# Kernel optimization log

Hardware: AMD Instinct MI355X
Metric: run time of the kernel (lower is better)

Reference implementation:

```python
import jax, jax.numpy as jnp
import numpy as np

BIAS = 1.0
SIGMA = 0.5
EPS = 1e-5


def mrf_loss(gen, target):
    # gen, target: [B, C, H, W]
    mean_t = jnp.mean(target, axis=1, keepdims=True)
    gf = gen - mean_t
    tf = target - mean_t
    gn = gf / jnp.linalg.norm(gf, axis=1, keepdims=True)
    tn = tf / jnp.linalg.norm(tf, axis=1, keepdims=True)
    B, C, H, W = target.shape
    # 1x1 patches of target, ordered by spatial position (matches unfold h,w order)
    patches = tn.transpose(0, 2, 3, 1).reshape(B, H * W, C)  # [B, P, C]
    # per-sample conv2d with 1x1 kernels == batched GEMM
    sim = jnp.einsum('bpc,bchw->bphw', patches, gn)  # [B, P, H, W]
    cosine_dist = -(sim - 1.0) / 2.0
    relative = cosine_dist / (jnp.min(cosine_dist, axis=1, keepdims=True) + EPS)
    dist = jnp.exp((BIAS - relative) / SIGMA)
    cs = dist / jnp.sum(dist, axis=1, keepdims=True)
    k_max = jnp.max(cs.reshape(B, H * W, -1), axis=2)  # [B, P]
    div_mrf = jnp.mean(k_max, axis=1)  # [B]
    return jnp.sum(-jnp.log(div_mrf))


def setup_inputs() -> dict:
    key = jax.random.key(0)
    k1, k2, k3, k4 = jax.random.split(key, 4)
    return {
        'gen_relu3_2': jax.random.normal(k1, (4, 256, 64, 64), dtype=jnp.float32),
        'tar_relu3_2': jax.random.normal(k2, (4, 256, 64, 64), dtype=jnp.float32),
        'gen_relu4_2': jax.random.normal(k3, (4, 512, 32, 32), dtype=jnp.float32),
        'tar_relu4_2': jax.random.normal(k4, (4, 512, 32, 32), dtype=jnp.float32),
    }


def reference(gen_relu3_2, tar_relu3_2, gen_relu4_2, tar_relu4_2):
    # style layers: relu3_2 (w=1.0), relu4_2 (w=1.0); content layers: relu4_2 (w=1.0)
    m3 = mrf_loss(gen_relu3_2, tar_relu3_2)
    m4 = mrf_loss(gen_relu4_2, tar_relu4_2)
    style_loss = (1.0 * m3 + 1.0 * m4) * 1.0  # l_s = 1.0
    content_loss = (1.0 * m4) * 1.0           # l_c = 1.0
    return style_loss + content_loss
```

## Files before the change

kernel.cpp:

```cpp
#include <hip/hip_runtime.h>
#include <math.h>


#define MRF_EPS 1e-5f
#define LOG2E 1.44269504088896340736f

typedef __attribute__((ext_vector_type(8))) short bf16x8;
typedef __attribute__((ext_vector_type(4))) float f32x4;
typedef unsigned short ushort_t;
struct __align__(8) ushort4_t { ushort_t x, y, z, w; };
struct __align__(16) ushort8_t { ushort_t v[8]; };

__device__ __forceinline__ ushort_t f2bf(float x) {
    unsigned u = __float_as_uint(x);
    u += 0x7FFFu + ((u >> 16) & 1u);
    return (ushort_t)(u >> 16);
}
__device__ __forceinline__ float bf2f(ushort_t u) {
    return __uint_as_float(((unsigned)u) << 16);
}

typedef __attribute__((address_space(1))) const unsigned int gu32;
typedef __attribute__((address_space(3))) unsigned int lu32;
__device__ __forceinline__ void gload16(const ushort_t* g, ushort_t* l) {
    __builtin_amdgcn_global_load_lds((gu32*)(uintptr_t)g, (lu32*)(uintptr_t)l,
                                     16, 0, 0);
}

__global__ __launch_bounds__(256) void stats_all(
    const float* __restrict__ gen3, const float* __restrict__ tar3,
    const float* __restrict__ gen4, const float* __restrict__ tar4,
    float* __restrict__ mean3, float* __restrict__ rg3, float* __restrict__ rt3,
    float* __restrict__ mean4, float* __restrict__ rg4, float* __restrict__ rt4) {
    const float *gen, *tar; float *mean, *rg, *rt; int C, S, b, bx;
    int bid = blockIdx.x;
    if (bid < 256) {
        C = 512; S = 1024; b = bid >> 6; bx = bid & 63;
        gen = gen4; tar = tar4; mean = mean4; rg = rg4; rt = rt4;
    } else {
        bid -= 256;
        C = 256; S = 4096; b = bid >> 8; bx = bid & 255;
        gen = gen3; tar = tar3; mean = mean3; rg = rg3; rt = rt3;
    }
    int tid = threadIdx.x, pq = tid & 3, cs = tid >> 2;
    int s0 = bx * 16 + pq * 4;
    const float* g = gen + (size_t)b * C * S + s0;
    const float* t = tar + (size_t)b * C * S + s0;

    f32x4 st = {0.f, 0.f, 0.f, 0.f}, st2 = st, sg = st, sg2 = st;
    for (int c = cs; c < C; c += 64) {
        f32x4 tv = *(const f32x4*)(t + (size_t)c * S);
        f32x4 gv = *(const f32x4*)(g + (size_t)c * S);
        st += tv; st2 += tv * tv; sg += gv; sg2 += gv * gv;
    }
    __shared__ f32x4 red[4][4][64];
    __shared__ f32x4 red2[4][4][4];
    red[0][pq][cs] = st; red[1][pq][cs] = st2; red[2][pq][cs] = sg; red[3][pq][cs] = sg2;
    __syncthreads();
    if (tid < 64) {
        int s_ = tid >> 4, p_ = (tid >> 2) & 3, part = tid & 3;
        f32x4 s = red[s_][p_][part * 16];
#pragma unroll
        for (int j = 1; j < 16; j++) s += red[s_][p_][part * 16 + j];
        red2[s_][p_][part] = s;
    }
    __syncthreads();
    if (tid < 4) {
        f32x4 sts = red2[0][tid][0] + red2[0][tid][1] + red2[0][tid][2] + red2[0][tid][3];
        f32x4 st2s = red2[1][tid][0] + red2[1][tid][1] + red2[1][tid][2] + red2[1][tid][3];
        f32x4 sgs = red2[2][tid][0] + red2[2][tid][1] + red2[2][tid][2] + red2[2][tid][3];
        f32x4 sg2s = red2[3][tid][0] + red2[3][tid][1] + red2[3][tid][2] + red2[3][tid][3];
        f32x4 m, vrt, vrg;
        float invC = 1.f / (float)C;
#pragma unroll
        for (int e = 0; e < 4; e++) {
            float mm = sts[e] * invC;
            m[e] = mm;
            vrt[e] = rsqrtf(st2s[e] - mm * sts[e]);
            vrg[e] = rsqrtf(sg2s[e] - 2.f * mm * sgs[e] + mm * sts[e]);
        }
        int idx = b * S + bx * 16 + tid * 4;
        *(f32x4*)(mean + idx) = m;
        *(f32x4*)(rt + idx) = vrt;
        *(f32x4*)(rg + idx) = vrg;
    }
}

__global__ __launch_bounds__(256) void apply_all(
    const float* __restrict__ gen3, const float* __restrict__ tar3,
    const float* __restrict__ gen4, const float* __restrict__ tar4,
    const float* __restrict__ mean3, const float* __restrict__ rg3, const float* __restrict__ rt3,
    const float* __restrict__ mean4, const float* __restrict__ rg4, const float* __restrict__ rt4,
    ushort_t* __restrict__ gnT3, ushort_t* __restrict__ tnT3,
    ushort_t* __restrict__ gnT4, ushort_t* __restrict__ tnT4) {
    const float *gen, *tar, *mean, *rg, *rt; ushort_t *gnT, *tnT;
    int C, S, b, sxb, cyb;
    int bid = blockIdx.x;
    if (bid < 512) {
        C = 512; S = 1024; b = bid >> 7; int rem = bid & 127;
        cyb = rem >> 4; sxb = rem & 15;
        gen = gen4; tar = tar4; mean = mean4; rg = rg4; rt = rt4; gnT = gnT4; tnT = tnT4;
    } else {
        bid -= 512;
        C = 256; S = 4096; b = bid >> 8; int rem = bid & 255;
        cyb = rem >> 6; sxb = rem & 63;
        gen = gen3; tar = tar3; mean = mean3; rg = rg3; rt = rt3; gnT = gnT3; tnT = tnT3;
    }
    int tid = threadIdx.x;
    int s0 = sxb * 64, c0 = cyb * 64;
    const float* g = gen + (size_t)b * C * S;
    const float* t = tar + (size_t)b * C * S;
    int tx = tid & 63, tw = tid >> 6;
    int sidx = b * S + s0 + tx;
    float m = mean[sidx], rgv = rg[sidx], rtv = rt[sidx];

    __shared__ ushort_t tg[64][72], tt_[64][72];
#pragma unroll
    for (int i = 0; i < 16; i++) {
        int cl = tw * 16 + i;
        float gv = g[(size_t)(c0 + cl) * S + s0 + tx];
        float tv = t[(size_t)(c0 + cl) * S + s0 + tx];
        tg[tx][cl] = f2bf((gv - m) * rgv);
        tt_[tx][cl] = f2bf((tv - m) * rtv);
    }
    __syncthreads();
    int KC = C >> 3;
#pragma unroll
    for (int j = 0; j < 2; j++) {
        int p = j * 256 + tid;
        int s = p & 63, ch = p >> 6;
        int row = s0 + s;
        int r16 = row >> 4, lm = row & 15;
        size_t off = (size_t)b * S * C + (((size_t)r16 * KC + (c0 >> 3) + ch) * 16 + lm) * 8;
        *(ushort8_t*)(gnT + off) = *(const ushort8_t*)&tg[s][ch * 8];
        *(ushort8_t*)(tnT + off) = *(const ushort8_t*)&tt_[s][ch * 8];
    }
}

template <int K>
__device__ __forceinline__ void gemm_body(
    const ushort_t* __restrict__ A, const ushort_t* __restrict__ B,
    ushort_t* __restrict__ sim, float* __restrict__ cmPart,
    int S, int bx, int by, ushort_t* __restrict__ lds) {
    const int tid = threadIdx.x;
    const int lane = tid & 63, wave = tid >> 6;
    const int wm = (wave & 1) * 64, wn = (wave >> 1) * 64;
    const int lm = lane & 15, quad = lane >> 4;
    const int q0 = bx * 128;

    constexpr int KC = K / 8;
    constexpr int KB = K / 32;

    const ushort_t* segsrc[4];
    ushort_t* segdst[4];
#pragma unroll
    for (int i = 0; i < 4; i++) {
        int s = wave * 4 + i;
        segsrc[i] = (s < 8)
            ? A + ((size_t)(by * 8 + s) * KC) * 128 + lane * 8
            : B + ((size_t)(bx * 8 + (s - 8)) * KC) * 128 + lane * 8;
        segdst[i] = lds + s * 512;
    }

    auto stage = [&](int buf, int kb) {
#pragma unroll
        for (int i = 0; i < 4; i++)
            gload16(segsrc[i] + (size_t)kb * 512, segdst[i] + buf * 8192);
    };

    f32x4 acc[4][4];
#pragma unroll
    for (int t = 0; t < 4; t++)
#pragma unroll
        for (int u = 0; u < 4; u++) acc[t][u] = (f32x4){0.f, 0.f, 0.f, 0.f};

    stage(0, 0);
    stage(1, 1);
    asm volatile("s_waitcnt vmcnt(4)" ::: "memory");
    __builtin_amdgcn_s_barrier();

    const ushort_t* lA = lds + (wm >> 4) * 512 + quad * 128 + lm * 8;
    const ushort_t* lB = lds + 4096 + (wn >> 4) * 512 + quad * 128 + lm * 8;

#pragma unroll
    for (int kb = 0; kb < KB; kb++) {
        const int cur = (kb % 3) * 8192;
        if (kb + 2 < KB) stage((kb + 2) % 3, kb + 2);
        bf16x8 a[4], b[4];
#pragma unroll
        for (int t = 0; t < 4; t++) {
            a[t] = *(const bf16x8*)(lA + cur + t * 512);
            b[t] = *(const bf16x8*)(lB + cur + t * 512);
        }
        asm volatile("s_waitcnt lgkmcnt(0)" ::: "memory");
        __builtin_amdgcn_sched_barrier(0);
#pragma unroll
        for (int t = 0; t < 4; t++)
#pragma unroll
            for (int u = 0; u < 4; u++)
                acc[t][u] = __builtin_amdgcn_mfma_f32_16x16x32_bf16(a[t], b[u], acc[t][u], 0, 0, 0);
        if (kb + 1 < KB) {
            if (kb + 2 < KB) asm volatile("s_waitcnt vmcnt(4)" ::: "memory");
            else             asm volatile("s_waitcnt vmcnt(0)" ::: "memory");
            __builtin_amdgcn_s_barrier();
        }
    }

    int nQB = S >> 7;
    size_t base = ((size_t)(by * nQB + bx)) * 16384
                + (size_t)(wave * 4096 + quad * 64 + lm * 4);
    float cmax[4] = {-INFINITY, -INFINITY, -INFINITY, -INFINITY};
#pragma unroll
    for (int t = 0; t < 4; t++)
#pragma unroll
        for (int u = 0; u < 4; u++) {
            f32x4 v = acc[t][u];
            ushort4_t o;
            o.x = f2bf(v.x); o.y = f2bf(v.y); o.z = f2bf(v.z); o.w = f2bf(v.w);
            *(ushort4_t*)(sim + base + (t * 4 + u) * 256) = o;
            float mx = fmaxf(fmaxf(bf2f(o.x), bf2f(o.y)), fmaxf(bf2f(o.z), bf2f(o.w)));
            cmax[u] = fmaxf(cmax[u], mx);
        }
    int r = by * 2 + (wave & 1);
#pragma unroll
    for (int u = 0; u < 4; u++) {
        float m = cmax[u];
        m = fmaxf(m, __shfl_xor(m, 16, 64));
        m = fmaxf(m, __shfl_xor(m, 32, 64));
        if (lane < 16) cmPart[(size_t)r * S + q0 + wn + u * 16 + lane] = m;
    }
}

__global__ __launch_bounds__(256) void gemm_all(
    const ushort_t* __restrict__ tnT3, const ushort_t* __restrict__ gnT3,
    ushort_t* __restrict__ sim3, float* __restrict__ cmPart3,
    const ushort_t* __restrict__ tnT4, const ushort_t* __restrict__ gnT4,
    ushort_t* __restrict__ sim4, float* __restrict__ cmPart4) {
    __shared__ ushort_t lds[24576];
    int bid = blockIdx.x;
    if (bid < 256) {
        int z = bid >> 6, rem = bid & 63, by = rem >> 3, bx = rem & 7;
        gemm_body<512>(tnT4 + (size_t)z * 524288, gnT4 + (size_t)z * 524288,
                       sim4 + (size_t)z * 1048576, cmPart4 + (size_t)z * 16384,
                       1024, bx, by, lds);
    } else {
        bid -= 256;
        int z = bid >> 10, rem = bid & 1023, by = rem >> 5, bx = rem & 31;
        gemm_body<256>(tnT3 + (size_t)z * 1048576, gnT3 + (size_t)z * 1048576,
                       sim3 + (size_t)z * 16777216, cmPart3 + (size_t)z * 262144,
                       4096, bx, by, lds);
    }
}

__global__ __launch_bounds__(256) void colmax_reduce_all(
    const float* __restrict__ cmPart3, float2* __restrict__ coef3, float* __restrict__ colsum3,
    const float* __restrict__ cmPart4, float2* __restrict__ coef4, float* __restrict__ colsum4,
    float* __restrict__ acc) {
    const float* cmPart; float2* coef; float* colsum; int S, R, qb, accIdx;
    int bid = blockIdx.x;
    if (bid < 16) {
        int z = bid >> 2; qb = bid & 3; S = 1024; R = 16; accIdx = 4 + z;
        cmPart = cmPart4 + (size_t)z * 16384; coef = coef4 + (size_t)z * 1024;
        colsum = colsum4 + (size_t)z * 1024;
    } else {
        bid -= 16;
        int z = bid >> 4; qb = bid & 15; S = 4096; R = 64; accIdx = z;
        cmPart = cmPart3 + (size_t)z * 262144; coef = coef3 + (size_t)z * 4096;
        colsum = colsum3 + (size_t)z * 4096;
    }
    if (qb == 0 && threadIdx.x == 0) acc[accIdx] = 0.f;
    int q = qb * 256 + threadIdx.x;
    float m = cmPart[q];
    for (int r = 1; r < R; r++) m = fmaxf(m, cmPart[(size_t)r * S + q]);
    float c1 = 1.f / ((1.f - m) * 0.5f + MRF_EPS);
    coef[q] = make_float2((2.f - c1) * LOG2E, c1 * LOG2E);
    colsum[q] = 0.f;
}

__global__ __launch_bounds__(256) void colsum_all(
    const ushort_t* __restrict__ sim3, const float2* __restrict__ coef3, float* __restrict__ colsum3,
    const ushort_t* __restrict__ sim4, const float2* __restrict__ coef4, float* __restrict__ colsum4) {
    const ushort_t* sim; const float2* coef; float* colsum; int S, bx, by;
    int bid = blockIdx.x;
    if (bid < 256) {
        int z = bid >> 6, rem = bid & 63; by = rem >> 3; bx = rem & 7; S = 1024;
        sim = sim4 + (size_t)z * 1048576; coef = coef4 + (size_t)z * 1024;
        colsum = colsum4 + (size_t)z * 1024;
    } else {
        bid -= 256;
        int z = bid >> 10, rem = bid & 1023; by = rem >> 5; bx = rem & 31; S = 4096;
        sim = sim3 + (size_t)z * 16777216; coef = coef3 + (size_t)z * 4096;
        colsum = colsum3 + (size_t)z * 4096;
    }
    int tid = threadIdx.x, lane = tid & 63;
    int u = lane >> 4, lm = lane & 15;
    int sub = (tid >> 6) & 1, cg = tid >> 7;
    int nQB = S >> 7;
    int q = bx * 128 + cg * 64 + u * 16 + lm;
    float2 cc = coef[q];
    float c0 = cc.x, c1 = cc.y;
    const ushort_t* base = sim + ((size_t)(by * nQB + bx)) * 16384
                         + (size_t)((sub | (cg << 1)) * 4096 + u * 256 + lm * 4);
    float s = 0.f;
#pragma unroll
    for (int t = 0; t < 4; t++)
#pragma unroll
        for (int quad = 0; quad < 4; quad++) {
            ushort4_t w = *(const ushort4_t*)(base + t * 1024 + quad * 64);
            s += exp2f(c0 + c1 * bf2f(w.x)) + exp2f(c0 + c1 * bf2f(w.y))
               + exp2f(c0 + c1 * bf2f(w.z)) + exp2f(c0 + c1 * bf2f(w.w));
        }
    atomicAdd(colsum + q, s);
}

__global__ __launch_bounds__(256) void rowmax_all(
    const ushort_t* __restrict__ sim3, const float2* __restrict__ coef3, const float* __restrict__ colsum3,
    const ushort_t* __restrict__ sim4, const float2* __restrict__ coef4, const float* __restrict__ colsum4,
    float* __restrict__ acc) {
    const ushort_t* sim; const float2* coef; const float* colsum;
    int S, blk; float* accSlot;
    int bid = blockIdx.x;
    if (bid < 1024) {
        int z = bid >> 8; blk = bid & 255; S = 4096; accSlot = acc + z;
        sim = sim3 + (size_t)z * 16777216; coef = coef3 + (size_t)z * 4096;
        colsum = colsum3 + (size_t)z * 4096;
    } else {
        bid -= 1024;
        int z = bid >> 6; blk = bid & 63; S = 1024; accSlot = acc + 4 + z;
        sim = sim4 + (size_t)z * 1048576; coef = coef4 + (size_t)z * 1024;
        colsum = colsum4 + (size_t)z * 1024;
    }
    int wave = threadIdx.x >> 6, lane = threadIdx.x & 63;
    int g = blk * 4 + wave;
    int by = g >> 5, rem = g & 31;
    int sub = rem >> 4, t = (rem >> 2) & 3, quad = rem & 3;
    int u = lane >> 4, lm = lane & 15;
    int nQB = S >> 7;
    f32x4 m = {-INFINITY, -INFINITY, -INFINITY, -INFINITY};
    for (int bx = 0; bx < nQB; bx++) {
#pragma unroll
        for (int cg = 0; cg < 2; cg++) {
            int q = bx * 128 + cg * 64 + u * 16 + lm;
            float2 cc = coef[q];
            float c0p = cc.x - log2f(colsum[q]);
            const ushort_t* ptr = sim + ((size_t)(by * nQB + bx)) * 16384
                                + (size_t)((sub | (cg << 1)) * 4096 + (t * 4 + u) * 256 + quad * 64 + lm * 4);
            ushort4_t w = *(const ushort4_t*)ptr;
            m[0] = fmaxf(m[0], c0p + cc.y * bf2f(w.x));
            m[1] = fmaxf(m[1], c0p + cc.y * bf2f(w.y));
            m[2] = fmaxf(m[2], c0p + cc.y * bf2f(w.z));
            m[3] = fmaxf(m[3], c0p + cc.y * bf2f(w.w));
        }
    }
#pragma unroll
    for (int off = 32; off >= 1; off >>= 1)
#pragma unroll
        for (int e = 0; e < 4; e++)
            m[e] = fmaxf(m[e], __shfl_xor(m[e], off, 64));
    __shared__ float partial[4];
    if (lane == 0)
        partial[wave] = exp2f(m[0]) + exp2f(m[1]) + exp2f(m[2]) + exp2f(m[3]);
    __syncthreads();
    if (threadIdx.x == 0)
        atomicAdd(accSlot, partial[0] + partial[1] + partial[2] + partial[3]);
}

__global__ void finalize_kernel(const float* __restrict__ acc, float* __restrict__ out) {
    float loss = 0.f;
    for (int b = 0; b < 4; b++) loss += -logf(acc[b] * (1.f / 4096.f));
    for (int b = 0; b < 4; b++) loss += -2.f * logf(acc[4 + b] * (1.f / 1024.f));
    out[0] = loss;
}

extern "C" void kernel_launch(void* const* d_in, const int* in_sizes, int n_in,
                              void* d_out, int out_size, void* d_ws, size_t ws_size,
                              hipStream_t stream) {
    const float* gen3 = (const float*)d_in[0];
    const float* tar3 = (const float*)d_in[1];
    const float* gen4 = (const float*)d_in[2];
    const float* tar4 = (const float*)d_in[3];

    char* wsb = (char*)d_ws;
    size_t off = 0;
    auto alloc = [&](size_t bytes) {
        void* p = wsb + off;
        off += (bytes + 255) & ~(size_t)255;
        return p;
    };
    ushort_t* sim3 = (ushort_t*)alloc((size_t)4 * 16777216 * 2);
    ushort_t* gnT3 = (ushort_t*)alloc((size_t)4 * 1048576 * 2);
    ushort_t* tnT3 = (ushort_t*)alloc((size_t)4 * 1048576 * 2);
    float* cmPart3 = (float*)alloc((size_t)4 * 262144 * 4);
    float2* coef3 = (float2*)alloc((size_t)4 * 4096 * 8);
    float* colsum3 = (float*)alloc((size_t)4 * 4096 * 4);
    float* mean3 = (float*)alloc((size_t)4 * 4096 * 4);
    float* rg3 = (float*)alloc((size_t)4 * 4096 * 4);
    float* rt3 = (float*)alloc((size_t)4 * 4096 * 4);
    ushort_t* sim4 = (ushort_t*)alloc((size_t)4 * 1048576 * 2);
    ushort_t* gnT4 = (ushort_t*)alloc((size_t)4 * 524288 * 2);
    ushort_t* tnT4 = (ushort_t*)alloc((size_t)4 * 524288 * 2);
    float* cmPart4 = (float*)alloc((size_t)4 * 16384 * 4);
    float2* coef4 = (float2*)alloc((size_t)4 * 1024 * 8);
    float* colsum4 = (float*)alloc((size_t)4 * 1024 * 4);
    float* mean4 = (float*)alloc((size_t)4 * 1024 * 4);
    float* rg4 = (float*)alloc((size_t)4 * 1024 * 4);
    float* rt4 = (float*)alloc((size_t)4 * 1024 * 4);
    float* acc = (float*)alloc(64 * 4);

    stats_all<<<256 + 1024, 256, 0, stream>>>(
        gen3, tar3, gen4, tar4, mean3, rg3, rt3, mean4, rg4, rt4);
    apply_all<<<512 + 1024, 256, 0, stream>>>(
        gen3, tar3, gen4, tar4, mean3, rg3, rt3, mean4, rg4, rt4,
        gnT3, tnT3, gnT4, tnT4);
    gemm_all<<<256 + 4096, 256, 0, stream>>>(
        tnT3, gnT3, sim3, cmPart3, tnT4, gnT4, sim4, cmPart4);
    colmax_reduce_all<<<16 + 64, 256, 0, stream>>>(
        cmPart3, coef3, colsum3, cmPart4, coef4, colsum4, acc);
    colsum_all<<<256 + 4096, 256, 0, stream>>>(
        sim3, coef3, colsum3, sim4, coef4, colsum4);
    rowmax_all<<<1024 + 256, 256, 0, stream>>>(
        sim3, coef3, colsum3, sim4, coef4, colsum4, acc);
    finalize_kernel<<<1, 1, 0, stream>>>(acc, (float*)d_out);
}
```

Before: 228.1 us.

## Recompute similarity GEMM in fused epilogues instead of materializing sim matrix

Removes the bf16 similarity buffer and instead reruns the batched GEMM three times: for column max, for the softmax column sums, and for per-tile row maxima. Row maxima go to a partial buffer that a small reduce kernel combines. This trades the large HBM write and two full re-reads of the similarity matrix for two extra passes of MFMA compute and on-chip epilogue work. Rounding to bf16 is kept so the values match the previous path.

Result: slower. 273.1 us (+19.7%).

```diff
diff --git a/kernel.cpp b/kernel.cpp
--- a/kernel.cpp
+++ b/kernel.cpp
@@ -19,6 +19,7 @@
 __device__ __forceinline__ float bf2f(ushort_t u) {
     return __uint_as_float(((unsigned)u) << 16);
 }
+__device__ __forceinline__ float rndbf(float x) { return bf2f(f2bf(x)); }
 
 typedef __attribute__((address_space(1))) const unsigned int gu32;
 typedef __attribute__((address_space(3))) unsigned int lu32;
@@ -138,15 +139,13 @@
 }
 
 template <int K>
-__device__ __forceinline__ void gemm_body(
+__device__ __forceinline__ void gemm_core(
     const ushort_t* __restrict__ A, const ushort_t* __restrict__ B,
-    ushort_t* __restrict__ sim, float* __restrict__ cmPart,
-    int S, int bx, int by, ushort_t* __restrict__ lds) {
+    int bx, int by, ushort_t* __restrict__ lds, f32x4 (&acc)[4][4]) {
     const int tid = threadIdx.x;
     const int lane = tid & 63, wave = tid >> 6;
     const int wm = (wave & 1) * 64, wn = (wave >> 1) * 64;
     const int lm = lane & 15, quad = lane >> 4;
-    const int q0 = bx * 128;
 
     constexpr int KC = K / 8;
     constexpr int KB = K / 32;
@@ -168,7 +167,6 @@
             gload16(segsrc[i] + (size_t)kb * 512, segdst[i] + buf * 8192);
     };
 
-    f32x4 acc[4][4];
 #pragma unroll
     for (int t = 0; t < 4; t++)
 #pragma unroll
@@ -205,20 +203,20 @@
             __builtin_amdgcn_s_barrier();
         }
     }
-
-    int nQB = S >> 7;
-    size_t base = ((size_t)(by * nQB + bx)) * 16384
-                + (size_t)(wave * 4096 + quad * 64 + lm * 4);
+}
+
+__device__ __forceinline__ void epilogueA(
+    f32x4 (&acc)[4][4], float* __restrict__ cmPart, int S, int bx, int by) {
+    int tid = threadIdx.x, lane = tid & 63, wave = tid >> 6;
+    int wn = (wave >> 1) * 64;
+    int q0 = bx * 128;
     float cmax[4] = {-INFINITY, -INFINITY, -INFINITY, -INFINITY};
 #pragma unroll
     for (int t = 0; t < 4; t++)
 #pragma unroll
         for (int u = 0; u < 4; u++) {
             f32x4 v = acc[t][u];
-            ushort4_t o;
-            o.x = f2bf(v.x); o.y = f2bf(v.y); o.z = f2bf(v.z); o.w = f2bf(v.w);
-            *(ushort4_t*)(sim + base + (t * 4 + u) * 256) = o;
-            float mx = fmaxf(fmaxf(bf2f(o.x), bf2f(o.y)), fmaxf(bf2f(o.z), bf2f(o.w)));
+            float mx = fmaxf(fmaxf(rndbf(v.x), rndbf(v.y)), fmaxf(rndbf(v.z), rndbf(v.w)));
             cmax[u] = fmaxf(cmax[u], mx);
         }
     int r = by * 2 + (wave & 1);
@@ -231,24 +229,23 @@
     }
 }
 
-__global__ __launch_bounds__(256) void gemm_all(
+__global__ __launch_bounds__(256) void gemmA_all(
     const ushort_t* __restrict__ tnT3, const ushort_t* __restrict__ gnT3,
-    ushort_t* __restrict__ sim3, float* __restrict__ cmPart3,
+    float* __restrict__ cmPart3,
     const ushort_t* __restrict__ tnT4, const ushort_t* __restrict__ gnT4,
-    ushort_t* __restrict__ sim4, float* __restrict__ cmPart4) {
+    float* __restrict__ cmPart4) {
     __shared__ ushort_t lds[24576];
+    f32x4 acc[4][4];
     int bid = blockIdx.x;
     if (bid < 256) {
         int z = bid >> 6, rem = bid & 63, by = rem >> 3, bx = rem & 7;
-        gemm_body<512>(tnT4 + (size_t)z * 524288, gnT4 + (size_t)z * 524288,
-                       sim4 + (size_t)z * 1048576, cmPart4 + (size_t)z * 16384,
-                       1024, bx, by, lds);
+        gemm_core<512>(tnT4 + (size_t)z * 524288, gnT4 + (size_t)z * 524288, bx, by, lds, acc);
+        epilogueA(acc, cmPart4 + (size_t)z * 16384, 1024, bx, by);
     } else {
         bid -= 256;
         int z = bid >> 10, rem = bid & 1023, by = rem >> 5, bx = rem & 31;
-        gemm_body<256>(tnT3 + (size_t)z * 1048576, gnT3 + (size_t)z * 1048576,
-                       sim3 + (size_t)z * 16777216, cmPart3 + (size_t)z * 262144,
-                       4096, bx, by, lds);
+        gemm_core<256>(tnT3 + (size_t)z * 1048576, gnT3 + (size_t)z * 1048576, bx, by, lds, acc);
+        epilogueA(acc, cmPart3 + (size_t)z * 262144, 4096, bx, by);
     }
 }
 
@@ -277,92 +274,157 @@
     colsum[q] = 0.f;
 }
 
-__global__ __launch_bounds__(256) void colsum_all(
-    const ushort_t* __restrict__ sim3, const float2* __restrict__ coef3, float* __restrict__ colsum3,
-    const ushort_t* __restrict__ sim4, const float2* __restrict__ coef4, float* __restrict__ colsum4) {
-    const ushort_t* sim; const float2* coef; float* colsum; int S, bx, by;
+__device__ __forceinline__ void epilogueB(
+    f32x4 (&acc)[4][4], const float2* __restrict__ coef,
+    float* __restrict__ colsum, int bx) {
+    int tid = threadIdx.x, lane = tid & 63, wave = tid >> 6;
+    int wn = (wave >> 1) * 64, lm = lane & 15;
+    int qb = bx * 128 + wn + lm;
+    float c0[4], c1[4], su[4];
+#pragma unroll
+    for (int u = 0; u < 4; u++) {
+        float2 cc = coef[qb + u * 16];
+        c0[u] = cc.x; c1[u] = cc.y; su[u] = 0.f;
+    }
+#pragma unroll
+    for (int t = 0; t < 4; t++)
+#pragma unroll
+        for (int u = 0; u < 4; u++) {
+            f32x4 v = acc[t][u];
+            su[u] += exp2f(c0[u] + c1[u] * rndbf(v.x));
+            su[u] += exp2f(c0[u] + c1[u] * rndbf(v.y));
+            su[u] += exp2f(c0[u] + c1[u] * rndbf(v.z));
+            su[u] += exp2f(c0[u] + c1[u] * rndbf(v.w));
+        }
+#pragma unroll
+    for (int u = 0; u < 4; u++) {
+        su[u] += __shfl_xor(su[u], 16, 64);
+        su[u] += __shfl_xor(su[u], 32, 64);
+        if (lane < 16) atomicAdd(colsum + qb + u * 16, su[u]);
+    }
+}
+
+__global__ __launch_bounds__(256) void gemmB_all(
+    const ushort_t* __restrict__ tnT3, const ushort_t* __restrict__ gnT3,
+    const float2* __restrict__ coef3, float* __restrict__ colsum3,
+    const ushort_t* __restrict__ tnT4, const ushort_t* __restrict__ gnT4,
+    const float2* __restrict__ coef4, float* __restrict__ colsum4) {
+    __shared__ ushort_t lds[24576];
+    f32x4 acc[4][4];
     int bid = blockIdx.x;
     if (bid < 256) {
-        int z = bid >> 6, rem = bid & 63; by = rem >> 3; bx = rem & 7; S = 1024;
-        sim = sim4 + (size_t)z * 1048576; coef = coef4 + (size_t)z * 1024;
-        colsum = colsum4 + (size_t)z * 1024;
+        int z = bid >> 6, rem = bid & 63, by = rem >> 3, bx = rem & 7;
+        gemm_core<512>(tnT4 + (size_t)z * 524288, gnT4 + (size_t)z * 524288, bx, by, lds, acc);
+        epilogueB(acc, coef4 + (size_t)z * 1024, colsum4 + (size_t)z * 1024, bx);
     } else {
         bid -= 256;
-        int z = bid >> 10, rem = bid & 1023; by = rem >> 5; bx = rem & 31; S = 4096;
-        sim = sim3 + (size_t)z * 16777216; coef = coef3 + (size_t)z * 4096;
-        colsum = colsum3 + (size_t)z * 4096;
-    }
-    int tid = threadIdx.x, lane = tid & 63;
-    int u = lane >> 4, lm = lane & 15;
-    int sub = (tid >> 6) & 1, cg = tid >> 7;
-    int nQB = S >> 7;
-    int q = bx * 128 + cg * 64 + u * 16 + lm;
-    float2 cc = coef[q];
-    float c0 = cc.x, c1 = cc.y;
-    const ushort_t* base = sim + ((size_t)(by * nQB + bx)) * 16384
-                         + (size_t)((sub | (cg << 1)) * 4096 + u * 256 + lm * 4);
-    float s = 0.f;
+        int z = bid >> 10, rem = bid & 1023, by = rem >> 5, bx = rem & 31;
+        gemm_core<256>(tnT3 + (size_t)z * 1048576, gnT3 + (size_t)z * 1048576, bx, by, lds, acc);
+        epilogueB(acc, coef3 + (size_t)z * 4096, colsum3 + (size_t)z * 4096, bx);
+    }
+}
+
+__device__ __forceinline__ void epilogueC(
+    f32x4 (&acc)[4][4], const float2* __restrict__ coef,
+    const float* __restrict__ colsum, float* __restrict__ rmPart,
+    int S, int bx, int by, float* __restrict__ rowm ) {
+    int tid = threadIdx.x, lane = tid & 63, wave = tid >> 6;
+    int wm = (wave & 1) * 64, wn = (wave >> 1) * 64;
+    int lm = lane & 15, quad = lane >> 4;
+    int qb = bx * 128 + wn + lm;
+    float c0p[4], c1[4];
+#pragma unroll
+    for (int u = 0; u < 4; u++) {
+        float2 cc = coef[qb + u * 16];
+        c0p[u] = cc.x - log2f(colsum[qb + u * 16]);
+        c1[u] = cc.y;
+    }
+    float m[4][4];
 #pragma unroll
     for (int t = 0; t < 4; t++)
 #pragma unroll
-        for (int quad = 0; quad < 4; quad++) {
-            ushort4_t w = *(const ushort4_t*)(base + t * 1024 + quad * 64);
-            s += exp2f(c0 + c1 * bf2f(w.x)) + exp2f(c0 + c1 * bf2f(w.y))
-               + exp2f(c0 + c1 * bf2f(w.z)) + exp2f(c0 + c1 * bf2f(w.w));
-        }
-    atomicAdd(colsum + q, s);
-}
-
-__global__ __launch_bounds__(256) void rowmax_all(
-    const ushort_t* __restrict__ sim3, const float2* __restrict__ coef3, const float* __restrict__ colsum3,
-    const ushort_t* __restrict__ sim4, const float2* __restrict__ coef4, const float* __restrict__ colsum4,
+        for (int r = 0; r < 4; r++) m[t][r] = -INFINITY;
+#pragma unroll
+    for (int t = 0; t < 4; t++)
+#pragma unroll
+        for (int u = 0; u < 4; u++) {
+            f32x4 v = acc[t][u];
+            m[t][0] = fmaxf(m[t][0], c0p[u] + c1[u] * rndbf(v.x));
+            m[t][1] = fmaxf(m[t][1], c0p[u] + c1[u] * rndbf(v.y));
+            m[t][2] = fmaxf(m[t][2], c0p[u] + c1[u] * rndbf(v.z));
+            m[t][3] = fmaxf(m[t][3], c0p[u] + c1[u] * rndbf(v.w));
+        }
+#pragma unroll
+    for (int off = 1; off <= 8; off <<= 1)
+#pragma unroll
+        for (int t = 0; t < 4; t++)
+#pragma unroll
+            for (int r = 0; r < 4; r++)
+                m[t][r] = fmaxf(m[t][r], __shfl_xor(m[t][r], off, 64));
+    __syncthreads();
+    if (lm == 0) {
+#pragma unroll
+        for (int t = 0; t < 4; t++)
+#pragma unroll
+            for (int r = 0; r < 4; r++)
+                rowm[(wave >> 1) * 128 + wm + t * 16 + quad * 4 + r] = m[t][r];
+    }
+    __syncthreads();
+    if (tid < 128) {
+        float v = fmaxf(rowm[tid], rowm[128 + tid]);
+        rmPart[(size_t)bx * S + by * 128 + tid] = v;
+    }
+}
+
+__global__ __launch_bounds__(256) void gemmC_all(
+    const ushort_t* __restrict__ tnT3, const ushort_t* __restrict__ gnT3,
+    const float2* __restrict__ coef3, const float* __restrict__ colsum3,
+    float* __restrict__ rmPart3,
+    const ushort_t* __restrict__ tnT4, const ushort_t* __restrict__ gnT4,
+    const float2* __restrict__ coef4, const float* __restrict__ colsum4,
+    float* __restrict__ rmPart4) {
+    __shared__ ushort_t lds[24576];
+    f32x4 acc[4][4];
+    int bid = blockIdx.x;
+    if (bid < 256) {
+        int z = bid >> 6, rem = bid & 63, by = rem >> 3, bx = rem & 7;
+        gemm_core<512>(tnT4 + (size_t)z * 524288, gnT4 + (size_t)z * 524288, bx, by, lds, acc);
+        epilogueC(acc, coef4 + (size_t)z * 1024, colsum4 + (size_t)z * 1024,
+                  rmPart4 + (size_t)z * 8192, 1024, bx, by, (float*)lds);
+    } else {
+        bid -= 256;
+        int z = bid >> 10, rem = bid & 1023, by = rem >> 5, bx = rem & 31;
+        gemm_core<256>(tnT3 + (size_t)z * 1048576, gnT3 + (size_t)z * 1048576, bx, by, lds, acc);
+        epilogueC(acc, coef3 + (size_t)z * 4096, colsum3 + (size_t)z * 4096,
+                  rmPart3 + (size_t)z * 131072, 4096, bx, by, (float*)lds);
+    }
+}
+
+__global__ __launch_bounds__(256) void rmreduce_all(
+    const float* __restrict__ rmPart3, const float* __restrict__ rmPart4,
     float* __restrict__ acc) {
-    const ushort_t* sim; const float2* coef; const float* colsum;
-    int S, blk; float* accSlot;
-    int bid = blockIdx.x;
-    if (bid < 1024) {
-        int z = bid >> 8; blk = bid & 255; S = 4096; accSlot = acc + z;
-        sim = sim3 + (size_t)z * 16777216; coef = coef3 + (size_t)z * 4096;
-        colsum = colsum3 + (size_t)z * 4096;
-    } else {
-        bid -= 1024;
-        int z = bid >> 6; blk = bid & 63; S = 1024; accSlot = acc + 4 + z;
-        sim = sim4 + (size_t)z * 1048576; coef = coef4 + (size_t)z * 1024;
-        colsum = colsum4 + (size_t)z * 1024;
-    }
-    int wave = threadIdx.x >> 6, lane = threadIdx.x & 63;
-    int g = blk * 4 + wave;
-    int by = g >> 5, rem = g & 31;
-    int sub = rem >> 4, t = (rem >> 2) & 3, quad = rem & 3;
-    int u = lane >> 4, lm = lane & 15;
-    int nQB = S >> 7;
-    f32x4 m = {-INFINITY, -INFINITY, -INFINITY, -INFINITY};
-    for (int bx = 0; bx < nQB; bx++) {
-#pragma unroll
-        for (int cg = 0; cg < 2; cg++) {
-            int q = bx * 128 + cg * 64 + u * 16 + lm;
-            float2 cc = coef[q];
-            float c0p = cc.x - log2f(colsum[q]);
-            const ushort_t* ptr = sim + ((size_t)(by * nQB + bx)) * 16384
-                                + (size_t)((sub | (cg << 1)) * 4096 + (t * 4 + u) * 256 + quad * 64 + lm * 4);
-            ushort4_t w = *(const ushort4_t*)ptr;
-            m[0] = fmaxf(m[0], c0p + cc.y * bf2f(w.x));
-            m[1] = fmaxf(m[1], c0p + cc.y * bf2f(w.y));
-            m[2] = fmaxf(m[2], c0p + cc.y * bf2f(w.z));
-            m[3] = fmaxf(m[3], c0p + cc.y * bf2f(w.w));
-        }
-    }
-#pragma unroll
-    for (int off = 32; off >= 1; off >>= 1)
-#pragma unroll
-        for (int e = 0; e < 4; e++)
-            m[e] = fmaxf(m[e], __shfl_xor(m[e], off, 64));
-    __shared__ float partial[4];
-    if (lane == 0)
-        partial[wave] = exp2f(m[0]) + exp2f(m[1]) + exp2f(m[2]) + exp2f(m[3]);
+    const float* rm; int S, nQB, p; float* slot;
+    int bid = blockIdx.x;
+    if (bid < 64) {
+        int z = bid >> 4, blk = bid & 15; S = 4096; nQB = 32;
+        rm = rmPart3 + (size_t)z * 131072;
+        p = blk * 256 + threadIdx.x; slot = acc + z;
+    } else {
+        bid -= 64;
+        int z = bid >> 2, blk = bid & 3; S = 1024; nQB = 8;
+        rm = rmPart4 + (size_t)z * 8192;
+        p = blk * 256 + threadIdx.x; slot = acc + 4 + z;
+    }
+    float m = rm[p];
+    for (int bx = 1; bx < nQB; bx++) m = fmaxf(m, rm[(size_t)bx * S + p]);
+    float k = exp2f(m);
+#pragma unroll
+    for (int off = 32; off >= 1; off >>= 1) k += __shfl_xor(k, off, 64);
+    __shared__ float part[4];
+    if ((threadIdx.x & 63) == 0) part[threadIdx.x >> 6] = k;
     __syncthreads();
     if (threadIdx.x == 0)
-        atomicAdd(accSlot, partial[0] + partial[1] + partial[2] + partial[3]);
+        atomicAdd(slot, part[0] + part[1] + part[2] + part[3]);
 }
 
 __global__ void finalize_kernel(const float* __restrict__ acc, float* __restrict__ out) {
@@ -387,21 +449,21 @@
         off += (bytes + 255) & ~(size_t)255;
         return p;
     };
-    ushort_t* sim3 = (ushort_t*)alloc((size_t)4 * 16777216 * 2);
     ushort_t* gnT3 = (ushort_t*)alloc((size_t)4 * 1048576 * 2);
     ushort_t* tnT3 = (ushort_t*)alloc((size_t)4 * 1048576 * 2);
     float* cmPart3 = (float*)alloc((size_t)4 * 262144 * 4);
     float2* coef3 = (float2*)alloc((size_t)4 * 4096 * 8);
     float* colsum3 = (float*)alloc((size_t)4 * 4096 * 4);
+    float* rmPart3 = (float*)alloc((size_t)4 * 131072 * 4);
     float* mean3 = (float*)alloc((size_t)4 * 4096 * 4);
     float* rg3 = (float*)alloc((size_t)4 * 4096 * 4);
     float* rt3 = (float*)alloc((size_t)4 * 4096 * 4);
-    ushort_t* sim4 = (ushort_t*)alloc((size_t)4 * 1048576 * 2);
     ushort_t* gnT4 = (ushort_t*)alloc((size_t)4 * 524288 * 2);
     ushort_t* tnT4 = (ushort_t*)alloc((size_t)4 * 524288 * 2);
     float* cmPart4 = (float*)alloc((size_t)4 * 16384 * 4);
     float2* coef4 = (float2*)alloc((size_t)4 * 1024 * 8);
     float* colsum4 = (float*)alloc((size_t)4 * 1024 * 4);
+    float* rmPart4 = (float*)alloc((size_t)4 * 8192 * 4);
     float* mean4 = (float*)alloc((size_t)4 * 1024 * 4);
     float* rg4 = (float*)alloc((size_t)4 * 1024 * 4);
     float* rt4 = (float*)alloc((size_t)4 * 1024 * 4);
@@ -412,13 +474,14 @@
     apply_all<<<512 + 1024, 256, 0, stream>>>(
         gen3, tar3, gen4, tar4, mean3, rg3, rt3, mean4, rg4, rt4,
         gnT3, tnT3, gnT4, tnT4);
-    gemm_all<<<256 + 4096, 256, 0, stream>>>(
-        tnT3, gnT3, sim3, cmPart3, tnT4, gnT4, sim4, cmPart4);
+    gemmA_all<<<256 + 4096, 256, 0, stream>>>(
+        tnT3, gnT3, cmPart3, tnT4, gnT4, cmPart4);
     colmax_reduce_all<<<16 + 64, 256, 0, stream>>>(
         cmPart3, coef3, colsum3, cmPart4, coef4, colsum4, acc);
-    colsum_all<<<256 + 4096, 256, 0, stream>>>(
-        sim3, coef3, colsum3, sim4, coef4, colsum4);
-    rowmax_all<<<1024 + 256, 256, 0, stream>>>(
-        sim3, coef3, colsum3, sim4, coef4, colsum4, acc);
+    gemmB_all<<<256 + 4096, 256, 0, stream>>>(
+        tnT3, gnT3, coef3, colsum3, tnT4, gnT4, coef4, colsum4);
+    gemmC_all<<<256 + 4096, 256, 0, stream>>>(
+        tnT3, gnT3, coef3, colsum3, rmPart3, tnT4, gnT4, coef4, colsum4, rmPart4);
+    rmreduce_all<<<64 + 16, 256, 0, stream>>>(rmPart3, rmPart4, acc);
     finalize_kernel<<<1, 1, 0, stream>>>(acc, (float*)d_out);
 }
```

## Fuse stats and normalize kernels into one prep pass; tweak GEMM scheduling

Applied to the files above, without the earlier changes.

Merges the per-pixel channel statistics kernel and the normalize/transpose-to-bf16 kernel into a single kernel. Each block keeps its loaded gen/target values in registers, computes the mean and inverse norms, then writes the packed bf16 tiles directly. This removes the second full read of the fp32 inputs, the mean/norm round trip through global memory and one launch, at the cost of more registers and a 33KB LDS tile. The GEMM inner loop also drops the explicit lgkmcnt wait and sched_barrier, and adds s_setprio around the MFMA block plus sched_barriers after the s_barrier calls.

Measured after the change: 219.1 us. -4.0%, faster.

```diff
diff --git a/kernel.cpp b/kernel.cpp
--- a/kernel.cpp
+++ b/kernel.cpp
@@ -27,49 +27,52 @@
                                      16, 0, 0);
 }
 
-__global__ __launch_bounds__(256) void stats_all(
-    const float* __restrict__ gen3, const float* __restrict__ tar3,
-    const float* __restrict__ gen4, const float* __restrict__ tar4,
-    float* __restrict__ mean3, float* __restrict__ rg3, float* __restrict__ rt3,
-    float* __restrict__ mean4, float* __restrict__ rg4, float* __restrict__ rt4) {
-    const float *gen, *tar; float *mean, *rg, *rt; int C, S, b, bx;
-    int bid = blockIdx.x;
-    if (bid < 256) {
-        C = 512; S = 1024; b = bid >> 6; bx = bid & 63;
-        gen = gen4; tar = tar4; mean = mean4; rg = rg4; rt = rt4;
-    } else {
-        bid -= 256;
-        C = 256; S = 4096; b = bid >> 8; bx = bid & 255;
-        gen = gen3; tar = tar3; mean = mean3; rg = rg3; rt = rt3;
-    }
-    int tid = threadIdx.x, pq = tid & 3, cs = tid >> 2;
-    int s0 = bx * 16 + pq * 4;
-    const float* g = gen + (size_t)b * C * S + s0;
-    const float* t = tar + (size_t)b * C * S + s0;
-
+template <int C>
+__device__ __forceinline__ void prep_body(
+    const float* __restrict__ gen, const float* __restrict__ tar,
+    ushort_t* __restrict__ gnT, ushort_t* __restrict__ tnT,
+    int S, int b, int bx, char* __restrict__ smem) {
+    constexpr int KN = C / 64;
+    constexpr int KC = C / 8;
+    constexpr int CP = C + 8;
+    const int tid = threadIdx.x, pq = tid & 3, cs = tid >> 2;
+    const int s0 = bx * 16;
+
+    f32x4* red  = (f32x4*)smem;
+    f32x4* red2 = (f32x4*)(smem + 16384);
+    ushort_t* tileG = (ushort_t*)smem;
+    ushort_t* tileT = tileG + 16 * CP;
+    float* sm  = (float*)(smem + 33280);
+    float* srt = sm + 16;
+    float* srg = sm + 32;
+
+    const float* g = gen + (size_t)b * C * S + s0 + pq * 4;
+    const float* t = tar + (size_t)b * C * S + s0 + pq * 4;
+
+    f32x4 gv[KN], tv[KN];
     f32x4 st = {0.f, 0.f, 0.f, 0.f}, st2 = st, sg = st, sg2 = st;
-    for (int c = cs; c < C; c += 64) {
-        f32x4 tv = *(const f32x4*)(t + (size_t)c * S);
-        f32x4 gv = *(const f32x4*)(g + (size_t)c * S);
-        st += tv; st2 += tv * tv; sg += gv; sg2 += gv * gv;
-    }
-    __shared__ f32x4 red[4][4][64];
-    __shared__ f32x4 red2[4][4][4];
-    red[0][pq][cs] = st; red[1][pq][cs] = st2; red[2][pq][cs] = sg; red[3][pq][cs] = sg2;
+#pragma unroll
+    for (int k = 0; k < KN; k++) {
+        tv[k] = *(const f32x4*)(t + (size_t)(cs + 64 * k) * S);
+        gv[k] = *(const f32x4*)(g + (size_t)(cs + 64 * k) * S);
+        st += tv[k]; st2 += tv[k] * tv[k]; sg += gv[k]; sg2 += gv[k] * gv[k];
+    }
+    red[(0 * 4 + pq) * 64 + cs] = st;  red[(1 * 4 + pq) * 64 + cs] = st2;
+    red[(2 * 4 + pq) * 64 + cs] = sg;  red[(3 * 4 + pq) * 64 + cs] = sg2;
     __syncthreads();
     if (tid < 64) {
         int s_ = tid >> 4, p_ = (tid >> 2) & 3, part = tid & 3;
-        f32x4 s = red[s_][p_][part * 16];
-#pragma unroll
-        for (int j = 1; j < 16; j++) s += red[s_][p_][part * 16 + j];
-        red2[s_][p_][part] = s;
+        f32x4 s = red[(s_ * 4 + p_) * 64 + part * 16];
+#pragma unroll
+        for (int j = 1; j < 16; j++) s += red[(s_ * 4 + p_) * 64 + part * 16 + j];
+        red2[(s_ * 4 + p_) * 4 + part] = s;
     }
     __syncthreads();
     if (tid < 4) {
-        f32x4 sts = red2[0][tid][0] + red2[0][tid][1] + red2[0][tid][2] + red2[0][tid][3];
-        f32x4 st2s = red2[1][tid][0] + red2[1][tid][1] + red2[1][tid][2] + red2[1][tid][3];
-        f32x4 sgs = red2[2][tid][0] + red2[2][tid][1] + red2[2][tid][2] + red2[2][tid][3];
-        f32x4 sg2s = red2[3][tid][0] + red2[3][tid][1] + red2[3][tid][2] + red2[3][tid][3];
+        f32x4 sts  = red2[(0*4+tid)*4+0] + red2[(0*4+tid)*4+1] + red2[(0*4+tid)*4+2] + red2[(0*4+tid)*4+3];
+        f32x4 st2s = red2[(1*4+tid)*4+0] + red2[(1*4+tid)*4+1] + red2[(1*4+tid)*4+2] + red2[(1*4+tid)*4+3];
+        f32x4 sgs  = red2[(2*4+tid)*4+0] + red2[(2*4+tid)*4+1] + red2[(2*4+tid)*4+2] + red2[(2*4+tid)*4+3];
+        f32x4 sg2s = red2[(3*4+tid)*4+0] + red2[(3*4+tid)*4+1] + red2[(3*4+tid)*4+2] + red2[(3*4+tid)*4+3];
         f32x4 m, vrt, vrg;
         float invC = 1.f / (float)C;
 #pragma unroll
@@ -79,61 +82,50 @@
             vrt[e] = rsqrtf(st2s[e] - mm * sts[e]);
             vrg[e] = rsqrtf(sg2s[e] - 2.f * mm * sgs[e] + mm * sts[e]);
         }
-        int idx = b * S + bx * 16 + tid * 4;
-        *(f32x4*)(mean + idx) = m;
-        *(f32x4*)(rt + idx) = vrt;
-        *(f32x4*)(rg + idx) = vrg;
-    }
-}
-
-__global__ __launch_bounds__(256) void apply_all(
+        *(f32x4*)&sm[tid * 4] = m;
+        *(f32x4*)&srt[tid * 4] = vrt;
+        *(f32x4*)&srg[tid * 4] = vrg;
+    }
+    __syncthreads();
+    f32x4 m4  = *(f32x4*)&sm[pq * 4];
+    f32x4 rt4 = *(f32x4*)&srt[pq * 4];
+    f32x4 rg4 = *(f32x4*)&srg[pq * 4];
+#pragma unroll
+    for (int k = 0; k < KN; k++) {
+        int c = cs + 64 * k;
+#pragma unroll
+        for (int e = 0; e < 4; e++) {
+            tileG[(pq * 4 + e) * CP + c] = f2bf((gv[k][e] - m4[e]) * rg4[e]);
+            tileT[(pq * 4 + e) * CP + c] = f2bf((tv[k][e] - m4[e]) * rt4[e]);
+        }
+    }
+    __syncthreads();
+    const int lm = tid & 15;
+    const int r16 = s0 >> 4;
+    size_t obase = (size_t)b * (size_t)S * C;
+#pragma unroll
+    for (int j = 0; j < KC / 16; j++) {
+        int ch = (tid >> 4) + 16 * j;
+        size_t off = obase + (((size_t)r16 * KC + ch) * 16 + lm) * 8;
+        *(ushort8_t*)(gnT + off) = *(const ushort8_t*)&tileG[lm * CP + ch * 8];
+        *(ushort8_t*)(tnT + off) = *(const ushort8_t*)&tileT[lm * CP + ch * 8];
+    }
+}
+
+__global__ __launch_bounds__(256) void prep_all(
     const float* __restrict__ gen3, const float* __restrict__ tar3,
     const float* __restrict__ gen4, const float* __restrict__ tar4,
-    const float* __restrict__ mean3, const float* __restrict__ rg3, const float* __restrict__ rt3,
-    const float* __restrict__ mean4, const float* __restrict__ rg4, const float* __restrict__ rt4,
     ushort_t* __restrict__ gnT3, ushort_t* __restrict__ tnT3,
     ushort_t* __restrict__ gnT4, ushort_t* __restrict__ tnT4) {
-    const float *gen, *tar, *mean, *rg, *rt; ushort_t *gnT, *tnT;
-    int C, S, b, sxb, cyb;
+    __shared__ __align__(16) char smem[33536];
     int bid = blockIdx.x;
-    if (bid < 512) {
-        C = 512; S = 1024; b = bid >> 7; int rem = bid & 127;
-        cyb = rem >> 4; sxb = rem & 15;
-        gen = gen4; tar = tar4; mean = mean4; rg = rg4; rt = rt4; gnT = gnT4; tnT = tnT4;
+    if (bid < 256) {
+        int z = bid >> 6, bx = bid & 63;
+        prep_body<512>(gen4, tar4, gnT4, tnT4, 1024, z, bx, smem);
     } else {
-        bid -= 512;
-        C = 256; S = 4096; b = bid >> 8; int rem = bid & 255;
-        cyb = rem >> 6; sxb = rem & 63;
-        gen = gen3; tar = tar3; mean = mean3; rg = rg3; rt = rt3; gnT = gnT3; tnT = tnT3;
-    }
-    int tid = threadIdx.x;
-    int s0 = sxb * 64, c0 = cyb * 64;
-    const float* g = gen + (size_t)b * C * S;
-    const float* t = tar + (size_t)b * C * S;
-    int tx = tid & 63, tw = tid >> 6;
-    int sidx = b * S + s0 + tx;
-    float m = mean[sidx], rgv = rg[sidx], rtv = rt[sidx];
-
-    __shared__ ushort_t tg[64][72], tt_[64][72];
-#pragma unroll
-    for (int i = 0; i < 16; i++) {
-        int cl = tw * 16 + i;
-        float gv = g[(size_t)(c0 + cl) * S + s0 + tx];
-        float tv = t[(size_t)(c0 + cl) * S + s0 + tx];
-        tg[tx][cl] = f2bf((gv - m) * rgv);
-        tt_[tx][cl] = f2bf((tv - m) * rtv);
-    }
-    __syncthreads();
-    int KC = C >> 3;
-#pragma unroll
-    for (int j = 0; j < 2; j++) {
-        int p = j * 256 + tid;
-        int s = p & 63, ch = p >> 6;
-        int row = s0 + s;
-        int r16 = row >> 4, lm = row & 15;
-        size_t off = (size_t)b * S * C + (((size_t)r16 * KC + (c0 >> 3) + ch) * 16 + lm) * 8;
-        *(ushort8_t*)(gnT + off) = *(const ushort8_t*)&tg[s][ch * 8];
-        *(ushort8_t*)(tnT + off) = *(const ushort8_t*)&tt_[s][ch * 8];
+        bid -= 256;
+        int z = bid >> 8, bx = bid & 255;
+        prep_body<256>(gen3, tar3, gnT3, tnT3, 4096, z, bx, smem);
     }
 }
 
@@ -178,6 +170,7 @@
     stage(1, 1);
     asm volatile("s_waitcnt vmcnt(4)" ::: "memory");
     __builtin_amdgcn_s_barrier();
+    __builtin_amdgcn_sched_barrier(0);
 
     const ushort_t* lA = lds + (wm >> 4) * 512 + quad * 128 + lm * 8;
     const ushort_t* lB = lds + 4096 + (wn >> 4) * 512 + quad * 128 + lm * 8;
@@ -192,17 +185,18 @@
             a[t] = *(const bf16x8*)(lA + cur + t * 512);
             b[t] = *(const bf16x8*)(lB + cur + t * 512);
         }
-        asm volatile("s_waitcnt lgkmcnt(0)" ::: "memory");
-        __builtin_amdgcn_sched_barrier(0);
+        __builtin_amdgcn_s_setprio(1);
 #pragma unroll
         for (int t = 0; t < 4; t++)
 #pragma unroll
             for (int u = 0; u < 4; u++)
                 acc[t][u] = __builtin_amdgcn_mfma_f32_16x16x32_bf16(a[t], b[u], acc[t][u], 0, 0, 0);
+        __builtin_amdgcn_s_setprio(0);
         if (kb + 1 < KB) {
             if (kb + 2 < KB) asm volatile("s_waitcnt vmcnt(4)" ::: "memory");
             else             asm volatile("s_waitcnt vmcnt(0)" ::: "memory");
             __builtin_amdgcn_s_barrier();
+            __builtin_amdgcn_sched_barrier(0);
         }
     }
 
@@ -393,25 +387,16 @@
     float* cmPart3 = (float*)alloc((size_t)4 * 262144 * 4);
     float2* coef3 = (float2*)alloc((size_t)4 * 4096 * 8);
     float* colsum3 = (float*)alloc((size_t)4 * 4096 * 4);
-    float* mean3 = (float*)alloc((size_t)4 * 4096 * 4);
-    float* rg3 = (float*)alloc((size_t)4 * 4096 * 4);
-    float* rt3 = (float*)alloc((size_t)4 * 4096 * 4);
     ushort_t* sim4 = (ushort_t*)alloc((size_t)4 * 1048576 * 2);
     ushort_t* gnT4 = (ushort_t*)alloc((size_t)4 * 524288 * 2);
     ushort_t* tnT4 = (ushort_t*)alloc((size_t)4 * 524288 * 2);
     float* cmPart4 = (float*)alloc((size_t)4 * 16384 * 4);
     float2* coef4 = (float2*)alloc((size_t)4 * 1024 * 8);
     float* colsum4 = (float*)alloc((size_t)4 * 1024 * 4);
-    float* mean4 = (float*)alloc((size_t)4 * 1024 * 4);
-    float* rg4 = (float*)alloc((size_t)4 * 1024 * 4);
-    float* rt4 = (float*)alloc((size_t)4 * 1024 * 4);
     float* acc = (float*)alloc(64 * 4);
 
-    stats_all<<<256 + 1024, 256, 0, stream>>>(
-        gen3, tar3, gen4, tar4, mean3, rg3, rt3, mean4, rg4, rt4);
-    apply_all<<<512 + 1024, 256, 0, stream>>>(
-        gen3, tar3, gen4, tar4, mean3, rg3, rt3, mean4, rg4, rt4,
-        gnT3, tnT3, gnT4, tnT4);
+    prep_all<<<256 + 1024, 256, 0, stream>>>(
+        gen3, tar3, gen4, tar4, gnT3, tnT3, gnT4, tnT4);
     gemm_all<<<256 + 4096, 256, 0, stream>>>(
         tnT3, gnT3, sim3, cmPart3, tnT4, gnT4, sim4, cmPart4);
     colmax_reduce_all<<<16 + 64, 256, 0, stream>>>(
```
